# Kernel tuning notes

Measured on AMD Instinct MI355X. Metric: run time of the kernel, lower is better.

Reference implementation:

```python
import jax, jax.numpy as jnp
import numpy as np

B, HH, WW = 8, 56, 56
N = HH * WW            # 3136 tokens
DIM, NH, SR = 512, 8, 7
HDIM = DIM // 2        # 256
LDIM = DIM - HDIM      # 256
DH = LDIM // NH        # 32
SCALE = DIM ** -0.5
EPS = 1e-5


def _dwconv(x, w):
    # depthwise 3x3, stride 1, SAME (= padding k//2): x [B,C,H,W], w [C,1,3,3]
    return jax.lax.conv_general_dilated(x, w, (1, 1), 'SAME',
                                        feature_group_count=x.shape[1],
                                        dimension_numbers=('NCHW', 'OIHW', 'NCHW'))


def _bn(x, g, b, m, v):
    # inference BatchNorm2d
    s = g * jax.lax.rsqrt(v + EPS)
    return (x - m[None, :, None, None]) * s[None, :, None, None] + b[None, :, None, None]


def _avg_pool(x, k):
    return jax.lax.reduce_window(x, 0.0, jax.lax.add, (1, 1, k, k), (1, 1, k, k), 'VALID') / (k * k)


def _max_pool(x, k):
    return jax.lax.reduce_window(x, -jnp.inf, jax.lax.max, (1, 1, k, k), (1, 1, k, k), 'VALID')


def setup_inputs() -> dict:
    key = jax.random.key(0)
    ks = jax.random.split(key, 32)
    d = {}
    d['x'] = jax.random.normal(ks[0], (B, N, DIM), jnp.float32)
    d['proj_v_w'] = jax.random.normal(ks[1], (LDIM, HDIM), jnp.float32) / np.sqrt(HDIM).astype(np.float32)
    d['conv1_w'] = jax.random.normal(ks[2], (LDIM, 1, 3, 3), jnp.float32) / 3.0
    d['conv2_w'] = jax.random.normal(ks[3], (LDIM, 1, 3, 3), jnp.float32) / 3.0
    d['conv3_w'] = jax.random.normal(ks[4], (HDIM, LDIM, 1, 1), jnp.float32) / np.sqrt(LDIM).astype(np.float32)
    d['conv3_b'] = jax.random.normal(ks[5], (HDIM,), jnp.float32) * 0.1
    d['v_conv_w'] = jax.random.normal(ks[6], (LDIM, 1, 3, 3), jnp.float32) / 3.0
    d['proj_w'] = jax.random.normal(ks[7], (DIM, DIM), jnp.float32) / np.sqrt(DIM).astype(np.float32)
    d['proj_b'] = jax.random.normal(ks[8], (DIM,), jnp.float32) * 0.1
    i = 9
    for pre, c in (('bn1', LDIM), ('bn2', LDIM), ('bn3', HDIM), ('vbn', LDIM)):
        d[pre + '_g'] = jax.random.uniform(ks[i], (c,), jnp.float32, 0.8, 1.2)
        d[pre + '_b'] = jax.random.normal(ks[i + 1], (c,), jnp.float32) * 0.1
        d[pre + '_m'] = jax.random.normal(ks[i + 2], (c,), jnp.float32) * 0.1
        d[pre + '_v'] = jax.random.uniform(ks[i + 3], (c,), jnp.float32, 0.5, 1.5)
        i += 4
    return d


def reference(x, proj_v_w, conv1_w, conv2_w, conv3_w, conv3_b, v_conv_w, proj_w, proj_b,
              bn1_g, bn1_b, bn1_m, bn1_v, bn2_g, bn2_b, bn2_m, bn2_v,
              bn3_g, bn3_b, bn3_m, bn3_v, vbn_g, vbn_b, vbn_m, vbn_v):
    x_high_in = x[..., :HDIM]                       # [B,N,HDIM]
    v = x_high_in @ proj_v_w.T                      # [B,N,LDIM]
    xh = v.reshape(B, HH, WW, LDIM).transpose(0, 3, 1, 2)   # [B,LDIM,H,W]
    xh = _bn(_dwconv(xh, conv1_w), bn1_g, bn1_b, bn1_m, bn1_v)
    q1 = _avg_pool(xh, SR)                          # [B,LDIM,8,8]
    q2 = _max_pool(xh, SR)
    xh = jax.nn.gelu(xh, approximate=False)
    xh = _bn(_dwconv(xh, conv2_w), bn2_g, bn2_b, bn2_m, bn2_v)
    k1 = _avg_pool(xh, SR)
    k2 = _max_pool(xh, SR)
    xh = jax.lax.conv_general_dilated(xh, conv3_w, (1, 1), 'SAME',
                                      dimension_numbers=('NCHW', 'OIHW', 'NCHW')) + conv3_b[None, :, None, None]
    xh = _bn(xh, bn3_g, bn3_b, bn3_m, bn3_v)
    xh = jax.nn.gelu(xh, approximate=False)
    x_high = xh.reshape(B, HDIM, N).transpose(0, 2, 1)      # [B,N,HDIM]

    hq, wq = HH // SR, WW // SR
    nq = hq * wq                                    # 64 pooled tokens

    def heads(t):                                   # [B,LDIM,hq,wq] -> [B,NH,nq,DH]
        return t.reshape(B, NH, DH, nq).transpose(0, 1, 3, 2)

    q = jnp.concatenate([heads(q1), heads(q2)], axis=-1)    # [B,NH,nq,2*DH]
    k = jnp.concatenate([heads(k1), heads(k2)], axis=-1)
    vh = v.reshape(B, N, NH, DH).transpose(0, 2, 1, 3)      # [B,NH,N,DH]

    attn = jnp.einsum('bhqd,bhkd->bhqk', q, k)              # [B,NH,nq,nq]
    attn = attn.reshape(B * NH, nq, hq, wq)
    attn = jax.image.resize(attn, (B * NH, nq, HH, WW), method='bilinear', antialias=False) * SCALE
    attn = attn.reshape(B, NH, nq, N)
    attn = jax.nn.softmax(attn, axis=-1)

    out = jnp.einsum('bhqn,bhnd->bhqd', attn, vh)           # [B,NH,nq,DH]
    out = out.reshape(B, NH, hq, wq, DH).transpose(0, 1, 4, 2, 3).reshape(B, LDIM, hq, wq)
    out = jax.image.resize(out, (B, LDIM, HH, WW), method='bilinear', antialias=False)
    out = _bn(_dwconv(out, v_conv_w), vbn_g, vbn_b, vbn_m, vbn_v)
    x_low = out.reshape(B, LDIM, N).transpose(0, 2, 1)      # [B,N,LDIM]

    y = jnp.concatenate([x_high, x_low], axis=-1) @ proj_w.T + proj_b
    return y
```

## Files before the change

kernel.cpp:

```cpp
#include <hip/hip_runtime.h>
#include <math.h>

#define BB 8
#define HH 56
#define WWD 56
#define NN 3136
#define CC 256
#define DIMM 512
#define NHEAD 8
#define NQ 64
#define EPSF 1e-5f
#define SCALEF 0.04419417382415922f

typedef __attribute__((ext_vector_type(8))) short short8;
typedef __attribute__((ext_vector_type(4))) float floatx4;

__device__ __forceinline__ float gelu_f(float x) {
    return 0.5f * x * (1.f + erff(x * 0.70710678118654752f));
}
__device__ __forceinline__ unsigned short f2bf(float f) {
    union { float f; unsigned u; } v; v.f = f;
    return (unsigned short)((v.u + 0x7fffu + ((v.u >> 16) & 1u)) >> 16);
}
__device__ __forceinline__ float bf2f(unsigned short u) {
    union { unsigned u; float f; } v; v.u = ((unsigned)u) << 16;
    return v.f;
}

__global__ __launch_bounds__(256) void cast3_k(
    const float* __restrict__ a, const float* __restrict__ b,
    const float* __restrict__ cc, unsigned short* __restrict__ da,
    unsigned short* __restrict__ db, unsigned short* __restrict__ dc) {
    int i = blockIdx.x * 256 + threadIdx.x;
    if (i < 65536) {
        da[i] = f2bf(a[i]);
        db[i] = f2bf(b[i]);
    }
    if (i < 262144) dc[i] = f2bf(cc[i]);
}

__global__ __launch_bounds__(256) void gemm_v_mfma(
    const float* __restrict__ x, const unsigned short* __restrict__ w16,
    unsigned short* __restrict__ v16) {
    __shared__ short Ws[128 * 72];
    __shared__ short Xs[128 * 72];
    int n0 = blockIdx.x * 128, c0 = blockIdx.y * 128;
    int tid = threadIdx.x;
    int lane = tid & 63, wv = tid >> 6;
    int wc = wv >> 1, wn = wv & 1;
    int quad = lane >> 4, l16 = lane & 15;
    floatx4 zero = {0.f, 0.f, 0.f, 0.f};
    floatx4 acc[4][4];
#pragma unroll
    for (int ci = 0; ci < 4; ci++)
#pragma unroll
        for (int ni = 0; ni < 4; ni++) acc[ci][ni] = zero;

    for (int k0 = 0; k0 < 256; k0 += 64) {
        {
            int m = tid >> 1;
            int ob = (tid & 1) * 4;
            const float* src = x + (size_t)(n0 + m) * DIMM + k0 + ob * 8;
            short* dst = &Xs[m * 72 + ob * 8];
#pragma unroll
            for (int i2 = 0; i2 < 4; i2++) {
                floatx4 f0 = *(const floatx4*)(src + i2 * 8);
                floatx4 f1 = *(const floatx4*)(src + i2 * 8 + 4);
                short8 pk;
                pk[0] = (short)f2bf(f0[0]); pk[1] = (short)f2bf(f0[1]);
                pk[2] = (short)f2bf(f0[2]); pk[3] = (short)f2bf(f0[3]);
                pk[4] = (short)f2bf(f1[0]); pk[5] = (short)f2bf(f1[1]);
                pk[6] = (short)f2bf(f1[2]); pk[7] = (short)f2bf(f1[3]);
                *(short8*)(dst + i2 * 8) = pk;
            }
        }
#pragma unroll
        for (int i2 = 0; i2 < 4; i2++) {
            int idx = tid + 256 * i2;
            int c = idx >> 3, o = idx & 7;
            *(short8*)&Ws[c * 72 + o * 8] =
                *(const short8*)(const short*)(w16 + (size_t)(c0 + c) * 256 + k0 + o * 8);
        }
        __syncthreads();
#pragma unroll
        for (int kc = 0; kc < 2; kc++) {
            short8 af[4], bf[4];
#pragma unroll
            for (int ci = 0; ci < 4; ci++)
                af[ci] = *(const short8*)&Ws[(wc * 64 + ci * 16 + l16) * 72 + (kc * 4 + quad) * 8];
#pragma unroll
            for (int ni = 0; ni < 4; ni++)
                bf[ni] = *(const short8*)&Xs[(wn * 64 + ni * 16 + l16) * 72 + (kc * 4 + quad) * 8];
#pragma unroll
            for (int ci = 0; ci < 4; ci++)
#pragma unroll
                for (int ni = 0; ni < 4; ni++)
                    acc[ci][ni] = __builtin_amdgcn_mfma_f32_16x16x32_bf16(
                        af[ci], bf[ni], acc[ci][ni], 0, 0, 0);
        }
        __syncthreads();
    }
#pragma unroll
    for (int ni = 0; ni < 4; ni++) {
        int ng = n0 + wn * 64 + ni * 16 + l16;
        int b = ng / NN, n = ng - b * NN;
#pragma unroll
        for (int ci = 0; ci < 4; ci++) {
#pragma unroll
            for (int r = 0; r < 4; r++) {
                int c = c0 + wc * 64 + ci * 16 + quad * 4 + r;
                v16[((size_t)b * CC + c) * NN + n] = f2bf(acc[ci][ni][r]);
            }
        }
    }
}

__device__ __forceinline__ float dw3x3(const float* __restrict__ Us, int i,
                                       float w0, float w1, float w2, float w3,
                                       float w4, float w5, float w6, float w7,
                                       float w8) {
    int y = i / 56, x = i - y * 56;
    bool ym = y > 0, yp = y < 55, xm = x > 0, xp = x < 55;
    const float* r1 = &Us[(y - 1) * 57 + x];
    const float* r2 = &Us[y * 57 + x];
    const float* r3 = &Us[(y + 1) * 57 + x];
    float acc = r2[0] * w4;
    if (xm) acc += r2[-1] * w3;
    if (xp) acc += r2[1] * w5;
    if (ym) {
        acc += r1[0] * w1;
        if (xm) acc += r1[-1] * w0;
        if (xp) acc += r1[1] * w2;
    }
    if (yp) {
        acc += r3[0] * w7;
        if (xm) acc += r3[-1] * w6;
        if (xp) acc += r3[1] * w8;
    }
    return acc;
}

__global__ __launch_bounds__(256) void dwconv2x_k(
    const unsigned short* __restrict__ in,
    const float* __restrict__ w1c, const float* __restrict__ g1,
    const float* __restrict__ b1, const float* __restrict__ m1,
    const float* __restrict__ v1,
    const float* __restrict__ w2c, const float* __restrict__ g2,
    const float* __restrict__ b2, const float* __restrict__ m2,
    const float* __restrict__ v2,
    unsigned short* __restrict__ out,
    float* __restrict__ oavg1, float* __restrict__ omax1,
    float* __restrict__ oavg2, float* __restrict__ omax2) {
    __shared__ float Us[56 * 57];
    __shared__ float Cs[NN];
    int bc = blockIdx.x;
    int c = bc & 255;
    int tid = threadIdx.x;
    const unsigned short* ip = in + (size_t)bc * NN;
    for (int i = tid; i < NN; i += 256) {
        int y = i / 56, x = i - y * 56;
        Us[y * 57 + x] = bf2f(ip[i]);
    }
    float w0 = w1c[c * 9 + 0], w1 = w1c[c * 9 + 1], w2 = w1c[c * 9 + 2];
    float w3 = w1c[c * 9 + 3], w4 = w1c[c * 9 + 4], w5 = w1c[c * 9 + 5];
    float w6 = w1c[c * 9 + 6], w7 = w1c[c * 9 + 7], w8 = w1c[c * 9 + 8];
    float s = g1[c] * rsqrtf(v1[c] + EPSF);
    float sh = b1[c] - m1[c] * s;
    __syncthreads();
    for (int i = tid; i < NN; i += 256)
        Cs[i] = dw3x3(Us, i, w0, w1, w2, w3, w4, w5, w6, w7, w8) * s + sh;
    __syncthreads();
    if (tid < 64) {
        int qy = tid >> 3, qx = tid & 7;
        const float* p0 = &Cs[(qy * 7) * 56 + qx * 7];
        float sm = 0.f, mx = -INFINITY;
#pragma unroll
        for (int py = 0; py < 7; py++)
#pragma unroll
            for (int px = 0; px < 7; px++) {
                float t = p0[py * 56 + px];
                sm += t;
                mx = fmaxf(mx, t);
            }
        oavg1[(size_t)bc * 64 + tid] = sm * (1.f / 49.f);
        omax1[(size_t)bc * 64 + tid] = mx;
    }
    for (int i = tid; i < NN; i += 256) {
        int y = i / 56, x = i - y * 56;
        Us[y * 57 + x] = gelu_f(Cs[i]);
    }
    w0 = w2c[c * 9 + 0]; w1 = w2c[c * 9 + 1]; w2 = w2c[c * 9 + 2];
    w3 = w2c[c * 9 + 3]; w4 = w2c[c * 9 + 4]; w5 = w2c[c * 9 + 5];
    w6 = w2c[c * 9 + 6]; w7 = w2c[c * 9 + 7]; w8 = w2c[c * 9 + 8];
    s = g2[c] * rsqrtf(v2[c] + EPSF);
    sh = b2[c] - m2[c] * s;
    __syncthreads();
    unsigned short* op = out + (size_t)bc * NN;
    for (int i = tid; i < NN; i += 256) {
        float val = dw3x3(Us, i, w0, w1, w2, w3, w4, w5, w6, w7, w8) * s + sh;
        Cs[i] = val;
        op[i] = f2bf(val);
    }
    __syncthreads();
    if (tid < 64) {
        int qy = tid >> 3, qx = tid & 7;
        const float* p0 = &Cs[(qy * 7) * 56 + qx * 7];
        float sm = 0.f, mx = -INFINITY;
#pragma unroll
        for (int py = 0; py < 7; py++)
#pragma unroll
            for (int px = 0; px < 7; px++) {
                float t = p0[py * 56 + px];
                sm += t;
                mx = fmaxf(mx, t);
            }
        oavg2[(size_t)bc * 64 + tid] = sm * (1.f / 49.f);
        omax2[(size_t)bc * 64 + tid] = mx;
    }
}

__global__ __launch_bounds__(256) void conv3_mfma(
    const unsigned short* __restrict__ xin, const unsigned short* __restrict__ w16,
    const float* __restrict__ bias, const float* __restrict__ g,
    const float* __restrict__ bparm, const float* __restrict__ mm,
    const float* __restrict__ vvv, unsigned short* __restrict__ out16) {
    __shared__ short As[128 * 72];
    __shared__ short Bs[128 * 72];
    int m0 = blockIdx.x * 128, c0 = blockIdx.y * 128;
    int tid = threadIdx.x;
    int lane = tid & 63, wv = tid >> 6;
    int wm = wv >> 1, wc = wv & 1;
    int quad = lane >> 4, l16 = lane & 15;
    floatx4 zero = {0.f, 0.f, 0.f, 0.f};
    floatx4 acc[4][4];
#pragma unroll
    for (int mi = 0; mi < 4; mi++)
#pragma unroll
        for (int ci = 0; ci < 4; ci++) acc[mi][ci] = zero;

    for (int k0 = 0; k0 < 256; k0 += 64) {
#pragma unroll
        for (int i2 = 0; i2 < 4; i2++) {
            int mo = i2 * 4 + wv;
            int kk = lane;
            int m8 = m0 + mo * 8;
            int b8 = m8 / NN, n8 = m8 - b8 * NN;
            short8 pk = *(const short8*)(const short*)(
                xin + ((size_t)b8 * CC + (k0 + kk)) * NN + n8);
            short* dst = &As[(mo * 8) * 72 + kk];
#pragma unroll
            for (int j = 0; j < 8; j++) dst[j * 72] = pk[j];
        }
#pragma unroll
        for (int i2 = 0; i2 < 4; i2++) {
            int idx = tid + 256 * i2;
            int c = idx >> 3, o = idx & 7;
            *(short8*)&Bs[c * 72 + o * 8] =
                *(const short8*)(const short*)(w16 + (size_t)(c0 + c) * CC + k0 + o * 8);
        }
        __syncthreads();
#pragma unroll
        for (int kc = 0; kc < 2; kc++) {
            short8 af[4], bf[4];
#pragma unroll
            for (int mi = 0; mi < 4; mi++)
                af[mi] = *(const short8*)&As[(wm * 64 + mi * 16 + l16) * 72 + (kc * 4 + quad) * 8];
#pragma unroll
            for (int ci = 0; ci < 4; ci++)
                bf[ci] = *(const short8*)&Bs[(wc * 64 + ci * 16 + l16) * 72 + (kc * 4 + quad) * 8];
#pragma unroll
            for (int mi = 0; mi < 4; mi++)
#pragma unroll
                for (int ci = 0; ci < 4; ci++)
                    acc[mi][ci] = __builtin_amdgcn_mfma_f32_16x16x32_bf16(
                        af[mi], bf[ci], acc[mi][ci], 0, 0, 0);
        }
        __syncthreads();
    }
#pragma unroll
    for (int ci = 0; ci < 4; ci++) {
        int co = c0 + wc * 64 + ci * 16 + l16;
        float s = g[co] * rsqrtf(vvv[co] + EPSF);
        float sh = bparm[co] - mm[co] * s;
        float bi = bias[co];
#pragma unroll
        for (int mi = 0; mi < 4; mi++) {
            int mbase = m0 + wm * 64 + mi * 16 + quad * 4;
#pragma unroll
            for (int r = 0; r < 4; r++) {
                float val = gelu_f((acc[mi][ci][r] + bi) * s + sh);
                out16[(size_t)(mbase + r) * CC + co] = f2bf(val);
            }
        }
    }
}

__global__ __launch_bounds__(256) void attn_qk_k(
    const float* __restrict__ q1, const float* __restrict__ q2,
    const float* __restrict__ k1, const float* __restrict__ k2,
    float* __restrict__ attn_s) {
    int b = blockIdx.x >> 3, h = blockIdx.x & 7;
    __shared__ float Qs[64][64];
    __shared__ float Ks[64][64];
    int tid = threadIdx.x;
#pragma unroll
    for (int l = 0; l < 16; l++) {
        int e = tid + 256 * l;
        int dt = e >> 6, i = e & 63;
        int d = dt & 31;
        const float* sq = (dt < 32) ? q1 : q2;
        const float* sk = (dt < 32) ? k1 : k2;
        Qs[dt][i] = sq[((size_t)b * CC + h * 32 + d) * NQ + i];
        Ks[dt][i] = sk[((size_t)b * CC + h * 32 + d) * NQ + i];
    }
    __syncthreads();
    int i = tid & 63, jg = tid >> 6;
    float acc[16] = {};
    for (int dt = 0; dt < 64; dt++) {
        float qv = Qs[dt][i];
#pragma unroll
        for (int t = 0; t < 16; t++) acc[t] += qv * Ks[dt][jg * 16 + t];
    }
    float* outp = attn_s + (((size_t)(b * 8 + h) * 64 + i) * 64) + jg * 16;
#pragma unroll
    for (int t = 0; t < 16; t++) outp[t] = acc[t];
}

__global__ __launch_bounds__(256) void attn_pv_k(
    const float* __restrict__ attn_s, const unsigned short* __restrict__ v16,
    float* __restrict__ part_O, float* __restrict__ part_rs) {
    __shared__ float asub[64][68];
    __shared__ float Mq[64];
    __shared__ unsigned short Vs[32][72];
    __shared__ short po4[64][4];
    __shared__ float pw4[64][4];
    int s = blockIdx.x, bh = blockIdx.y;
    int b = bh >> 3, h = bh & 7;
    int tid = threadIdx.x;
    int lane = tid & 63, wv = tid >> 6;
    int quad = lane >> 4, l16 = lane & 15;
    {
        int q = tid & 63, jg = tid >> 6;
        const float* src = attn_s + ((size_t)bh * 64 + q) * 64 + jg * 16;
        float* dst = &asub[q][jg * 16];
#pragma unroll
        for (int t = 0; t < 4; t++) {
            floatx4 f = *(const floatx4*)(src + t * 4);
            f[0] *= SCALEF; f[1] *= SCALEF; f[2] *= SCALEF; f[3] *= SCALEF;
            *(floatx4*)(dst + t * 4) = f;
        }
    }
    __syncthreads();
    if (tid < 64) {
        float mx = asub[tid][0];
        for (int j = 1; j < 64; j++) mx = fmaxf(mx, asub[tid][j]);
        Mq[tid] = mx;
    }
    __syncthreads();
    int q = wv * 16 + l16;
    float Mv = Mq[q];
    floatx4 zero = {0.f, 0.f, 0.f, 0.f};
    floatx4 acc0 = zero, acc1 = zero;
    float rsum = 0.f;
    for (int cch = 0; cch < 7; cch++) {
        int n0 = (s * 7 + cch) * 64;
        {
            int d = tid >> 3, part = tid & 7;
            *(short8*)&Vs[d][part * 8] =
                *(const short8*)(const short*)(v16 +
                    ((size_t)(b * CC + h * 32 + d)) * NN + n0 + part * 8);
        }
        if (tid < 64) {
            int n = n0 + tid;
            int oy = n / WWD, ox = n - oy * WWD;
            float sy = (oy + 0.5f) * 0.14285714285714285f - 0.5f;
            float sx = (ox + 0.5f) * 0.14285714285714285f - 0.5f;
            float fy0 = floorf(sy), fx0 = floorf(sx);
            int y0 = (int)fy0, x0 = (int)fx0;
            float fy = sy - fy0, fx = sx - fx0;
            int y0c = max(y0, 0), y1c = min(y0 + 1, 7);
            int x0c = max(x0, 0), x1c = min(x0 + 1, 7);
            po4[tid][0] = (short)(y0c * 8 + x0c);
            po4[tid][1] = (short)(y0c * 8 + x1c);
            po4[tid][2] = (short)(y1c * 8 + x0c);
            po4[tid][3] = (short)(y1c * 8 + x1c);
            pw4[tid][0] = (1.f - fy) * (1.f - fx);
            pw4[tid][1] = (1.f - fy) * fx;
            pw4[tid][2] = fy * (1.f - fx);
            pw4[tid][3] = fy * fx;
        }
        __syncthreads();
#pragma unroll
        for (int kc = 0; kc < 2; kc++) {
            short8 af;
#pragma unroll
            for (int j = 0; j < 8; j++) {
                int np = kc * 32 + quad * 8 + j;
                float val = pw4[np][0] * asub[q][po4[np][0]]
                          + pw4[np][1] * asub[q][po4[np][1]]
                          + pw4[np][2] * asub[q][po4[np][2]]
                          + pw4[np][3] * asub[q][po4[np][3]];
                float p = exp2f((val - Mv) * 1.44269504f);
                rsum += p;
                af[j] = (short)f2bf(p);
            }
            short8 bf0 = *(const short8*)&Vs[l16][kc * 32 + quad * 8];
            short8 bf1 = *(const short8*)&Vs[16 + l16][kc * 32 + quad * 8];
            acc0 = __builtin_amdgcn_mfma_f32_16x16x32_bf16(af, bf0, acc0, 0, 0, 0);
            acc1 = __builtin_amdgcn_mfma_f32_16x16x32_bf16(af, bf1, acc1, 0, 0, 0);
        }
        __syncthreads();
    }
    rsum += __shfl_xor(rsum, 16, 64);
    rsum += __shfl_xor(rsum, 32, 64);
    size_t base = ((size_t)bh * 7 + s) * 64;
    if (lane < 16) part_rs[base + wv * 16 + lane] = rsum;
#pragma unroll
    for (int nt = 0; nt < 2; nt++) {
        floatx4 a = nt ? acc1 : acc0;
#pragma unroll
        for (int r = 0; r < 4; r++) {
            int qo = wv * 16 + quad * 4 + r;
            part_O[(base + qo) * 32 + nt * 16 + l16] = a[r];
        }
    }
}

__global__ __launch_bounds__(256) void upconv_k(
    const float* __restrict__ part_O, const float* __restrict__ part_rs,
    const float* __restrict__ w,
    const float* __restrict__ g, const float* __restrict__ bparm,
    const float* __restrict__ m, const float* __restrict__ v,
    unsigned short* __restrict__ xlow16) {
    __shared__ float ts[64];
    __shared__ float Us[56 * 57];
    int bc = blockIdx.x;
    int c = bc & 255;
    int tid = threadIdx.x;
    if (tid < 64) {
        int h = c >> 5, d = c & 31;
        int bh = (bc >> 8) * 8 + h;
        float o = 0.f, rs = 0.f;
        for (int s7 = 0; s7 < 7; s7++) {
            size_t base = ((size_t)bh * 7 + s7) * 64 + tid;
            o += part_O[base * 32 + d];
            rs += part_rs[base];
        }
        ts[tid] = o / rs;
    }
    __syncthreads();
    for (int i = tid; i < NN; i += 256) {
        int y = i / 56, x = i - y * 56;
        float sy = (y + 0.5f) * 0.14285714285714285f - 0.5f;
        float sx = (x + 0.5f) * 0.14285714285714285f - 0.5f;
        float fy0 = floorf(sy), fx0 = floorf(sx);
        int y0 = (int)fy0, x0 = (int)fx0;
        float fy = sy - fy0, fx = sx - fx0;
        int y0c = max(y0, 0), y1c = min(y0 + 1, 7);
        int x0c = max(x0, 0), x1c = min(x0 + 1, 7);
        float v00 = ts[y0c * 8 + x0c], v01 = ts[y0c * 8 + x1c];
        float v10 = ts[y1c * 8 + x0c], v11 = ts[y1c * 8 + x1c];
        Us[y * 57 + x] = (1.f - fy) * ((1.f - fx) * v00 + fx * v01) +
                         fy * ((1.f - fx) * v10 + fx * v11);
    }
    float w0 = w[c * 9 + 0], w1 = w[c * 9 + 1], w2 = w[c * 9 + 2];
    float w3 = w[c * 9 + 3], w4 = w[c * 9 + 4], w5 = w[c * 9 + 5];
    float w6 = w[c * 9 + 6], w7 = w[c * 9 + 7], w8 = w[c * 9 + 8];
    float s = g[c] * rsqrtf(v[c] + EPSF);
    float sh = bparm[c] - m[c] * s;
    __syncthreads();
    unsigned short* op = xlow16 + (size_t)bc * NN;
    for (int i = tid; i < NN; i += 256)
        op[i] = f2bf(dw3x3(Us, i, w0, w1, w2, w3, w4, w5, w6, w7, w8) * s + sh);
}

__global__ __launch_bounds__(256) void proj_mfma(
    const unsigned short* __restrict__ xh16, const unsigned short* __restrict__ xl16,
    const unsigned short* __restrict__ w16, const float* __restrict__ bias,
    float* __restrict__ y) {
    __shared__ short As[128 * 72];
    __shared__ short Bs[128 * 72];
    int m0 = blockIdx.x * 128, c0 = blockIdx.y * 128;
    int tid = threadIdx.x;
    int lane = tid & 63, wv = tid >> 6;
    int wm = wv >> 1, wc = wv & 1;
    int quad = lane >> 4, l16 = lane & 15;
    floatx4 zero = {0.f, 0.f, 0.f, 0.f};
    floatx4 acc[4][4];
#pragma unroll
    for (int mi = 0; mi < 4; mi++)
#pragma unroll
        for (int ci = 0; ci < 4; ci++) acc[mi][ci] = zero;

    for (int k0 = 0; k0 < 512; k0 += 64) {
        if (k0 < 256) {
#pragma unroll
            for (int i2 = 0; i2 < 4; i2++) {
                int idx = tid + 256 * i2;
                int m = idx >> 3, o = idx & 7;
                *(short8*)&As[m * 72 + o * 8] =
                    *(const short8*)(const short*)(xh16 + (size_t)(m0 + m) * CC + k0 + o * 8);
            }
        } else {
#pragma unroll
            for (int i2 = 0; i2 < 4; i2++) {
                int mo = i2 * 4 + wv;
                int kk = lane;
                int m8 = m0 + mo * 8;
                int b8 = m8 / NN, n8 = m8 - b8 * NN;
                short8 pk = *(const short8*)(const short*)(
                    xl16 + ((size_t)b8 * CC + (k0 - 256 + kk)) * NN + n8);
                short* dst = &As[(mo * 8) * 72 + kk];
#pragma unroll
                for (int j = 0; j < 8; j++) dst[j * 72] = pk[j];
            }
        }
#pragma unroll
        for (int i2 = 0; i2 < 4; i2++) {
            int idx = tid + 256 * i2;
            int c = idx >> 3, o = idx & 7;
            *(short8*)&Bs[c * 72 + o * 8] =
                *(const short8*)(const short*)(w16 + (size_t)(c0 + c) * DIMM + k0 + o * 8);
        }
        __syncthreads();
#pragma unroll
        for (int kc = 0; kc < 2; kc++) {
            short8 af[4], bf[4];
#pragma unroll
            for (int mi = 0; mi < 4; mi++)
                af[mi] = *(const short8*)&As[(wm * 64 + mi * 16 + l16) * 72 + (kc * 4 + quad) * 8];
#pragma unroll
            for (int ci = 0; ci < 4; ci++)
                bf[ci] = *(const short8*)&Bs[(wc * 64 + ci * 16 + l16) * 72 + (kc * 4 + quad) * 8];
#pragma unroll
            for (int mi = 0; mi < 4; mi++)
#pragma unroll
                for (int ci = 0; ci < 4; ci++)
                    acc[mi][ci] = __builtin_amdgcn_mfma_f32_16x16x32_bf16(
                        af[mi], bf[ci], acc[mi][ci], 0, 0, 0);
        }
        __syncthreads();
    }
#pragma unroll
    for (int mi = 0; mi < 4; mi++) {
        int mbase = m0 + wm * 64 + mi * 16 + quad * 4;
#pragma unroll
        for (int ci = 0; ci < 4; ci++) {
            int co = c0 + wc * 64 + ci * 16 + l16;
            float bi = bias[co];
#pragma unroll
            for (int r = 0; r < 4; r++)
                y[(size_t)(mbase + r) * DIMM + co] = acc[mi][ci][r] + bi;
        }
    }
}

extern "C" void kernel_launch(void* const* d_in, const int* in_sizes, int n_in,
                              void* d_out, int out_size, void* d_ws, size_t ws_size,
                              hipStream_t stream) {
    const float* x        = (const float*)d_in[0];
    const float* proj_v_w = (const float*)d_in[1];
    const float* conv1_w  = (const float*)d_in[2];
    const float* conv2_w  = (const float*)d_in[3];
    const float* conv3_w  = (const float*)d_in[4];
    const float* conv3_b  = (const float*)d_in[5];
    const float* v_conv_w = (const float*)d_in[6];
    const float* proj_w   = (const float*)d_in[7];
    const float* proj_b   = (const float*)d_in[8];
    const float* bn1_g = (const float*)d_in[9],  *bn1_b = (const float*)d_in[10];
    const float* bn1_m = (const float*)d_in[11], *bn1_v = (const float*)d_in[12];
    const float* bn2_g = (const float*)d_in[13], *bn2_b = (const float*)d_in[14];
    const float* bn2_m = (const float*)d_in[15], *bn2_v = (const float*)d_in[16];
    const float* bn3_g = (const float*)d_in[17], *bn3_b = (const float*)d_in[18];
    const float* bn3_m = (const float*)d_in[19], *bn3_v = (const float*)d_in[20];
    const float* vbn_g = (const float*)d_in[21], *vbn_b = (const float*)d_in[22];
    const float* vbn_m = (const float*)d_in[23], *vbn_v = (const float*)d_in[24];

    const size_t big = (size_t)BB * CC * NN;
    unsigned short* v16    = (unsigned short*)d_ws;
    unsigned short* bufA16 = v16 + big;
    unsigned short* bufB16 = bufA16 + big;
    unsigned short* xh16   = bufB16 + big;
    unsigned short* xlow16 = xh16 + big;
    float* small = (float*)(xlow16 + big);
    float* q1 = small;
    float* q2 = q1 + (size_t)BB * CC * NQ;
    float* k1 = q2 + (size_t)BB * CC * NQ;
    float* k2 = k1 + (size_t)BB * CC * NQ;
    float* attn_s = k2 + (size_t)BB * CC * NQ;
    float* out_s  = attn_s + (size_t)BB * NHEAD * NQ * NQ;
    float* part_O = out_s + (size_t)BB * CC * NQ;
    float* part_rs = part_O + (size_t)64 * 7 * 64 * 32;
    unsigned short* w16v  = (unsigned short*)(part_rs + 64 * 7 * 64);
    unsigned short* w16c3 = w16v + 65536;
    unsigned short* w16p  = w16c3 + 65536;

    cast3_k<<<1024, 256, 0, stream>>>(proj_v_w, conv3_w, proj_w, w16v, w16c3, w16p);

    gemm_v_mfma<<<dim3(196, 2), 256, 0, stream>>>(x, w16v, v16);
    dwconv2x_k<<<BB * CC, 256, 0, stream>>>(
        v16, conv1_w, bn1_g, bn1_b, bn1_m, bn1_v,
        conv2_w, bn2_g, bn2_b, bn2_m, bn2_v, bufB16, q1, q2, k1, k2);
    conv3_mfma<<<dim3(196, 2), 256, 0, stream>>>(bufB16, w16c3, conv3_b,
                                                 bn3_g, bn3_b, bn3_m, bn3_v, xh16);
    attn_qk_k<<<64, 256, 0, stream>>>(q1, q2, k1, k2, attn_s);
    attn_pv_k<<<dim3(7, 64), 256, 0, stream>>>(attn_s, v16, part_O, part_rs);
    upconv_k<<<BB * CC, 256, 0, stream>>>(part_O, part_rs, v_conv_w,
                                          vbn_g, vbn_b, vbn_m, vbn_v, xlow16);
    proj_mfma<<<dim3(196, 4), 256, 0, stream>>>(xh16, xlow16, w16p, proj_b, (float*)d_out);
}
```

Baseline: 284.4 us.

## Split depthwise conv kernels into row chunks, approximate GELU, preload V tiles

The dual depthwise-conv kernel and the upsample-conv kernel now each launch four blocks per channel. Each block handles 14 output rows with a halo, which shrinks shared memory and raises parallelism and occupancy, at the cost of recomputing halo rows for the first conv. Exact erf in GELU is replaced by the Abramowitz-Stegun polynomial approximation, which introduces a small numerical error. The PV attention kernel loads its whole 448-token V slab and the interpolation tables once up front, removing the per-chunk syncs at the cost of more shared memory per block.

```diff
diff --git a/kernel.cpp b/kernel.cpp
--- a/kernel.cpp
+++ b/kernel.cpp
@@ -13,10 +13,19 @@
 #define SCALEF 0.04419417382415922f
 
 typedef __attribute__((ext_vector_type(8))) short short8;
+typedef __attribute__((ext_vector_type(4))) short short4v;
 typedef __attribute__((ext_vector_type(4))) float floatx4;
 
 __device__ __forceinline__ float gelu_f(float x) {
-    return 0.5f * x * (1.f + erff(x * 0.70710678118654752f));
+    float z = x * 0.70710678118654752f;
+    float a = fabsf(z);
+    float t = __builtin_amdgcn_rcpf(1.f + 0.3275911f * a);
+    float p = t * (0.254829592f + t * (-0.284496736f + t * (1.421413741f +
+              t * (-1.453152027f + t * 1.061405429f))));
+    float e = exp2f(-1.44269504f * a * a);
+    float erfa = 1.f - p * e;
+    float erfz = copysignf(erfa, z);
+    return 0.5f * x * (1.f + erfz);
 }
 __device__ __forceinline__ unsigned short f2bf(float f) {
     union { float f; unsigned u; } v; v.f = f;
@@ -115,15 +124,15 @@
     }
 }
 
-__device__ __forceinline__ float dw3x3(const float* __restrict__ Us, int i,
-                                       float w0, float w1, float w2, float w3,
-                                       float w4, float w5, float w6, float w7,
-                                       float w8) {
-    int y = i / 56, x = i - y * 56;
-    bool ym = y > 0, yp = y < 55, xm = x > 0, xp = x < 55;
-    const float* r1 = &Us[(y - 1) * 57 + x];
-    const float* r2 = &Us[y * 57 + x];
-    const float* r3 = &Us[(y + 1) * 57 + x];
+__device__ __forceinline__ float dw3x3g(const float* __restrict__ Us, int lr,
+                                        int x, bool ym, bool yp,
+                                        float w0, float w1, float w2, float w3,
+                                        float w4, float w5, float w6, float w7,
+                                        float w8) {
+    bool xm = x > 0, xp = x < 55;
+    const float* r1 = &Us[(lr - 1) * 57 + x];
+    const float* r2 = &Us[lr * 57 + x];
+    const float* r3 = &Us[(lr + 1) * 57 + x];
     float acc = r2[0] * w4;
     if (xm) acc += r2[-1] * w3;
     if (xp) acc += r2[1] * w5;
@@ -151,15 +160,30 @@
     unsigned short* __restrict__ out,
     float* __restrict__ oavg1, float* __restrict__ omax1,
     float* __restrict__ oavg2, float* __restrict__ omax2) {
-    __shared__ float Us[56 * 57];
-    __shared__ float Cs[NN];
-    int bc = blockIdx.x;
+    __shared__ float Us[18 * 57];
+    __shared__ float Cs[16 * 57];
+    int bid = blockIdx.x;
+    int bc = bid >> 2, chunk = bid & 3;
     int c = bc & 255;
+    int r0 = chunk * 14;
     int tid = threadIdx.x;
     const unsigned short* ip = in + (size_t)bc * NN;
-    for (int i = tid; i < NN; i += 256) {
-        int y = i / 56, x = i - y * 56;
-        Us[y * 57 + x] = bf2f(ip[i]);
+
+    int gl0 = max(r0 - 2, 0), gh0 = min(r0 + 15, 55);
+    int nin = (gh0 - gl0 + 1) * 56;
+    const unsigned short* ipb = ip + gl0 * 56;
+    {
+        int e = tid * 4;
+        if (e < nin) {
+            short4v pk = *(const short4v*)(const short*)(ipb + e);
+#pragma unroll
+            for (int j = 0; j < 4; j++) {
+                int el = e + j;
+                int ry = el / 56, x = el - ry * 56;
+                int lr = (gl0 + ry) - (r0 - 2);
+                Us[lr * 57 + x] = bf2f((unsigned short)pk[j]);
+            }
+        }
     }
     float w0 = w1c[c * 9 + 0], w1 = w1c[c * 9 + 1], w2 = w1c[c * 9 + 2];
     float w3 = w1c[c * 9 + 3], w4 = w1c[c * 9 + 4], w5 = w1c[c * 9 + 5];
@@ -167,27 +191,36 @@
     float s = g1[c] * rsqrtf(v1[c] + EPSF);
     float sh = b1[c] - m1[c] * s;
     __syncthreads();
-    for (int i = tid; i < NN; i += 256)
-        Cs[i] = dw3x3(Us, i, w0, w1, w2, w3, w4, w5, w6, w7, w8) * s + sh;
-    __syncthreads();
-    if (tid < 64) {
-        int qy = tid >> 3, qx = tid & 7;
-        const float* p0 = &Cs[(qy * 7) * 56 + qx * 7];
+    int c1lo = max(r0 - 1, 0), c1hi = min(r0 + 14, 55);
+    int n1 = (c1hi - c1lo + 1) * 56;
+    for (int i = tid; i < n1; i += 256) {
+        int ry = i / 56, x = i - ry * 56;
+        int gr = c1lo + ry;
+        int liu = gr - (r0 - 2);
+        float acc = dw3x3g(Us, liu, x, gr > 0, gr < 55,
+                           w0, w1, w2, w3, w4, w5, w6, w7, w8);
+        Cs[(gr - (r0 - 1)) * 57 + x] = acc * s + sh;
+    }
+    __syncthreads();
+    if (tid < 16) {
+        int qy = 2 * chunk + (tid >> 3), qx = tid & 7;
+        const float* p0 = &Cs[(qy * 7 - (r0 - 1)) * 57 + qx * 7];
         float sm = 0.f, mx = -INFINITY;
 #pragma unroll
         for (int py = 0; py < 7; py++)
 #pragma unroll
             for (int px = 0; px < 7; px++) {
-                float t = p0[py * 56 + px];
+                float t = p0[py * 57 + px];
                 sm += t;
                 mx = fmaxf(mx, t);
             }
-        oavg1[(size_t)bc * 64 + tid] = sm * (1.f / 49.f);
-        omax1[(size_t)bc * 64 + tid] = mx;
-    }
-    for (int i = tid; i < NN; i += 256) {
-        int y = i / 56, x = i - y * 56;
-        Us[y * 57 + x] = gelu_f(Cs[i]);
+        oavg1[(size_t)bc * 64 + qy * 8 + qx] = sm * (1.f / 49.f);
+        omax1[(size_t)bc * 64 + qy * 8 + qx] = mx;
+    }
+    for (int i = tid; i < n1; i += 256) {
+        int ry = i / 56, x = i - ry * 56;
+        int lr1 = (c1lo + ry) - (r0 - 1);
+        Us[lr1 * 57 + x] = gelu_f(Cs[lr1 * 57 + x]);
     }
     w0 = w2c[c * 9 + 0]; w1 = w2c[c * 9 + 1]; w2 = w2c[c * 9 + 2];
     w3 = w2c[c * 9 + 3]; w4 = w2c[c * 9 + 4]; w5 = w2c[c * 9 + 5];
@@ -196,26 +229,30 @@
     sh = b2[c] - m2[c] * s;
     __syncthreads();
     unsigned short* op = out + (size_t)bc * NN;
-    for (int i = tid; i < NN; i += 256) {
-        float val = dw3x3(Us, i, w0, w1, w2, w3, w4, w5, w6, w7, w8) * s + sh;
-        Cs[i] = val;
-        op[i] = f2bf(val);
-    }
-    __syncthreads();
-    if (tid < 64) {
-        int qy = tid >> 3, qx = tid & 7;
-        const float* p0 = &Cs[(qy * 7) * 56 + qx * 7];
+    for (int i = tid; i < 14 * 56; i += 256) {
+        int ry = i / 56, x = i - ry * 56;
+        int gr = r0 + ry;
+        int lg = ry + 1;
+        float val = dw3x3g(Us, lg, x, gr > 0, gr < 55,
+                           w0, w1, w2, w3, w4, w5, w6, w7, w8) * s + sh;
+        Cs[ry * 57 + x] = val;
+        op[gr * 56 + x] = f2bf(val);
+    }
+    __syncthreads();
+    if (tid < 16) {
+        int qy = 2 * chunk + (tid >> 3), qx = tid & 7;
+        const float* p0 = &Cs[((qy * 7) - r0) * 57 + qx * 7];
         float sm = 0.f, mx = -INFINITY;
 #pragma unroll
         for (int py = 0; py < 7; py++)
 #pragma unroll
             for (int px = 0; px < 7; px++) {
-                float t = p0[py * 56 + px];
+                float t = p0[py * 57 + px];
                 sm += t;
                 mx = fmaxf(mx, t);
             }
-        oavg2[(size_t)bc * 64 + tid] = sm * (1.f / 49.f);
-        omax2[(size_t)bc * 64 + tid] = mx;
+        oavg2[(size_t)bc * 64 + qy * 8 + qx] = sm * (1.f / 49.f);
+        omax2[(size_t)bc * 64 + qy * 8 + qx] = mx;
     }
 }
 
@@ -331,9 +368,9 @@
     float* __restrict__ part_O, float* __restrict__ part_rs) {
     __shared__ float asub[64][68];
     __shared__ float Mq[64];
-    __shared__ unsigned short Vs[32][72];
-    __shared__ short po4[64][4];
-    __shared__ float pw4[64][4];
+    __shared__ unsigned short Vs[32][456];
+    __shared__ short po4[448][4];
+    __shared__ float pw4[448][4];
     int s = blockIdx.x, bh = blockIdx.y;
     int b = bh >> 3, h = bh & 7;
     int tid = threadIdx.x;
@@ -350,6 +387,35 @@
             *(floatx4*)(dst + t * 4) = f;
         }
     }
+    {
+        int d = tid >> 3, o0 = tid & 7;
+        const unsigned short* vp =
+            v16 + ((size_t)(b * CC + h * 32 + d)) * NN + s * 448;
+#pragma unroll
+        for (int t = 0; t < 7; t++) {
+            int oc = o0 + t * 8;
+            *(short8*)&Vs[d][oc * 8] = *(const short8*)(const short*)(vp + oc * 8);
+        }
+    }
+    for (int idx = tid; idx < 448; idx += 256) {
+        int n = s * 448 + idx;
+        int oy = n / WWD, ox = n - oy * WWD;
+        float sy = (oy + 0.5f) * 0.14285714285714285f - 0.5f;
+        float sx = (ox + 0.5f) * 0.14285714285714285f - 0.5f;
+        float fy0 = floorf(sy), fx0 = floorf(sx);
+        int y0 = (int)fy0, x0 = (int)fx0;
+        float fy = sy - fy0, fx = sx - fx0;
+        int y0c = max(y0, 0), y1c = min(y0 + 1, 7);
+        int x0c = max(x0, 0), x1c = min(x0 + 1, 7);
+        po4[idx][0] = (short)(y0c * 8 + x0c);
+        po4[idx][1] = (short)(y0c * 8 + x1c);
+        po4[idx][2] = (short)(y1c * 8 + x0c);
+        po4[idx][3] = (short)(y1c * 8 + x1c);
+        pw4[idx][0] = (1.f - fy) * (1.f - fx);
+        pw4[idx][1] = (1.f - fy) * fx;
+        pw4[idx][2] = fy * (1.f - fx);
+        pw4[idx][3] = fy * fx;
+    }
     __syncthreads();
     if (tid < 64) {
         float mx = asub[tid][0];
@@ -363,39 +429,13 @@
     floatx4 acc0 = zero, acc1 = zero;
     float rsum = 0.f;
     for (int cch = 0; cch < 7; cch++) {
-        int n0 = (s * 7 + cch) * 64;
-        {
-            int d = tid >> 3, part = tid & 7;
-            *(short8*)&Vs[d][part * 8] =
-                *(const short8*)(const short*)(v16 +
-                    ((size_t)(b * CC + h * 32 + d)) * NN + n0 + part * 8);
-        }
-        if (tid < 64) {
-            int n = n0 + tid;
-            int oy = n / WWD, ox = n - oy * WWD;
-            float sy = (oy + 0.5f) * 0.14285714285714285f - 0.5f;
-            float sx = (ox + 0.5f) * 0.14285714285714285f - 0.5f;
-            float fy0 = floorf(sy), fx0 = floorf(sx);
-            int y0 = (int)fy0, x0 = (int)fx0;
-            float fy = sy - fy0, fx = sx - fx0;
-            int y0c = max(y0, 0), y1c = min(y0 + 1, 7);
-            int x0c = max(x0, 0), x1c = min(x0 + 1, 7);
-            po4[tid][0] = (short)(y0c * 8 + x0c);
-            po4[tid][1] = (short)(y0c * 8 + x1c);
-            po4[tid][2] = (short)(y1c * 8 + x0c);
-            po4[tid][3] = (short)(y1c * 8 + x1c);
-            pw4[tid][0] = (1.f - fy) * (1.f - fx);
-            pw4[tid][1] = (1.f - fy) * fx;
-            pw4[tid][2] = fy * (1.f - fx);
-            pw4[tid][3] = fy * fx;
-        }
-        __syncthreads();
 #pragma unroll
         for (int kc = 0; kc < 2; kc++) {
+            int col = cch * 64 + kc * 32 + quad * 8;
             short8 af;
 #pragma unroll
             for (int j = 0; j < 8; j++) {
-                int np = kc * 32 + quad * 8 + j;
+                int np = col + j;
                 float val = pw4[np][0] * asub[q][po4[np][0]]
                           + pw4[np][1] * asub[q][po4[np][1]]
                           + pw4[np][2] * asub[q][po4[np][2]]
@@ -404,12 +444,11 @@
                 rsum += p;
                 af[j] = (short)f2bf(p);
             }
-            short8 bf0 = *(const short8*)&Vs[l16][kc * 32 + quad * 8];
-            short8 bf1 = *(const short8*)&Vs[16 + l16][kc * 32 + quad * 8];
+            short8 bf0 = *(const short8*)&Vs[l16][col];
+            short8 bf1 = *(const short8*)&Vs[16 + l16][col];
             acc0 = __builtin_amdgcn_mfma_f32_16x16x32_bf16(af, bf0, acc0, 0, 0, 0);
             acc1 = __builtin_amdgcn_mfma_f32_16x16x32_bf16(af, bf1, acc1, 0, 0, 0);
         }
-        __syncthreads();
     }
     rsum += __shfl_xor(rsum, 16, 64);
     rsum += __shfl_xor(rsum, 32, 64);
@@ -433,9 +472,11 @@
     const float* __restrict__ m, const float* __restrict__ v,
     unsigned short* __restrict__ xlow16) {
     __shared__ float ts[64];
-    __shared__ float Us[56 * 57];
-    int bc = blockIdx.x;
+    __shared__ float Us[16 * 57];
+    int bid = blockIdx.x;
+    int bc = bid >> 2, chunk = bid & 3;
     int c = bc & 255;
+    int r0 = chunk * 14;
     int tid = threadIdx.x;
     if (tid < 64) {
         int h = c >> 5, d = c & 31;
@@ -449,9 +490,12 @@
         ts[tid] = o / rs;
     }
     __syncthreads();
-    for (int i = tid; i < NN; i += 256) {
-        int y = i / 56, x = i - y * 56;
-        float sy = (y + 0.5f) * 0.14285714285714285f - 0.5f;
+    int blo = max(r0 - 1, 0), bhi = min(r0 + 14, 55);
+    int nb = (bhi - blo + 1) * 56;
+    for (int i = tid; i < nb; i += 256) {
+        int ry = i / 56, x = i - ry * 56;
+        int gr = blo + ry;
+        float sy = (gr + 0.5f) * 0.14285714285714285f - 0.5f;
         float sx = (x + 0.5f) * 0.14285714285714285f - 0.5f;
         float fy0 = floorf(sy), fx0 = floorf(sx);
         int y0 = (int)fy0, x0 = (int)fx0;
@@ -460,8 +504,9 @@
         int x0c = max(x0, 0), x1c = min(x0 + 1, 7);
         float v00 = ts[y0c * 8 + x0c], v01 = ts[y0c * 8 + x1c];
         float v10 = ts[y1c * 8 + x0c], v11 = ts[y1c * 8 + x1c];
-        Us[y * 57 + x] = (1.f - fy) * ((1.f - fx) * v00 + fx * v01) +
-                         fy * ((1.f - fx) * v10 + fx * v11);
+        Us[(gr - (r0 - 1)) * 57 + x] =
+            (1.f - fy) * ((1.f - fx) * v00 + fx * v01) +
+            fy * ((1.f - fx) * v10 + fx * v11);
     }
     float w0 = w[c * 9 + 0], w1 = w[c * 9 + 1], w2 = w[c * 9 + 2];
     float w3 = w[c * 9 + 3], w4 = w[c * 9 + 4], w5 = w[c * 9 + 5];
@@ -470,8 +515,13 @@
     float sh = bparm[c] - m[c] * s;
     __syncthreads();
     unsigned short* op = xlow16 + (size_t)bc * NN;
-    for (int i = tid; i < NN; i += 256)
-        op[i] = f2bf(dw3x3(Us, i, w0, w1, w2, w3, w4, w5, w6, w7, w8) * s + sh);
+    for (int i = tid; i < 14 * 56; i += 256) {
+        int ry = i / 56, x = i - ry * 56;
+        int gr = r0 + ry;
+        float val = dw3x3g(Us, ry + 1, x, gr > 0, gr < 55,
+                           w0, w1, w2, w3, w4, w5, w6, w7, w8);
+        op[gr * 56 + x] = f2bf(val * s + sh);
+    }
 }
 
 __global__ __launch_bounds__(256) void proj_mfma(
@@ -598,14 +648,14 @@
     cast3_k<<<1024, 256, 0, stream>>>(proj_v_w, conv3_w, proj_w, w16v, w16c3, w16p);
 
     gemm_v_mfma<<<dim3(196, 2), 256, 0, stream>>>(x, w16v, v16);
-    dwconv2x_k<<<BB * CC, 256, 0, stream>>>(
+    dwconv2x_k<<<BB * CC * 4, 256, 0, stream>>>(
         v16, conv1_w, bn1_g, bn1_b, bn1_m, bn1_v,
         conv2_w, bn2_g, bn2_b, bn2_m, bn2_v, bufB16, q1, q2, k1, k2);
     conv3_mfma<<<dim3(196, 2), 256, 0, stream>>>(bufB16, w16c3, conv3_b,
                                                  bn3_g, bn3_b, bn3_m, bn3_v, xh16);
     attn_qk_k<<<64, 256, 0, stream>>>(q1, q2, k1, k2, attn_s);
     attn_pv_k<<<dim3(7, 64), 256, 0, stream>>>(attn_s, v16, part_O, part_rs);
-    upconv_k<<<BB * CC, 256, 0, stream>>>(part_O, part_rs, v_conv_w,
-                                          vbn_g, vbn_b, vbn_m, vbn_v, xlow16);
+    upconv_k<<<BB * CC * 4, 256, 0, stream>>>(part_O, part_rs, v_conv_w,
+                                              vbn_g, vbn_b, vbn_m, vbn_v, xlow16);
     proj_mfma<<<dim3(196, 4), 256, 0, stream>>>(xh16, xlow16, w16p, proj_b, (float*)d_out);
 }
```

Measured after the change: 265.9 us. 6.5% less time.
